# Optimization experiments

Hardware: AMD Instinct MI355X
Metric: run time of the kernel (lower is better)

Reference implementation:

```python
import math
import jax, jax.numpy as jnp
import numpy as np

# Neuron / simulation constants (from docstring defaults)
THETA = 10.0
TAU_SR = 10.0
TAU_REF = 1.0
SCALE_REF = 2.0
SCALE_RHO = 1.0
TS = 1.0
T_SAMPLE = 300


def _alpha_kernel(tau, mult, eps_tol):
    # Faithful to slayer._calculateAlphaKernel: eps(t) = mult * t/tau * exp(1 - t/tau),
    # truncated once |eps| < eps_tol and t > tau.
    vals = []
    for t in np.arange(0.0, T_SAMPLE, TS):
        v = mult * t / tau * math.exp(1.0 - t / tau)
        if abs(v) < eps_tol and t > tau:
            break
        vals.append(v)
    return np.asarray(vals, np.float32)


def psp(spike, srm_kernel):
    # slayerCuda.conv: causal temporal convolution psp[t] = sum_k f[k] * spike[t-k]
    N, C, H, W, T = spike.shape
    x = spike.reshape(-1, 1, T)                       # (B,1,T), B = N*C*H*W
    K = srm_kernel.shape[0]
    w = jnp.flip(srm_kernel).reshape(1, 1, K).astype(x.dtype)
    y = jax.lax.conv_general_dilated(
        x, w, window_strides=(1,), padding=[(K - 1, 0)],
        dimension_numbers=('NCH', 'OIH', 'NCH'))
    return y.reshape(N, C, H, W, T)


def get_spikes(u2, ref_kernel):
    # slayerCuda.getSpikes: sequential scan over time. At each step the effective
    # membrane potential is u[t] plus pending refractory contributions from past
    # spikes; a spike (value 1/Ts) fires when u_eff >= theta and injects the
    # refractory kernel into future timesteps.
    # u2: (B, T); ref_kernel: (K,) with ref_kernel[0] == 0 (alpha kernel).
    B, T = u2.shape
    K = ref_kernel.shape[0]
    ref_tail = ref_kernel[1:].astype(u2.dtype)        # contributions to t+1..t+K-1

    def step(pend, u_t):
        u_eff = u_t + pend[:, 0]
        s = (u_eff >= THETA).astype(u2.dtype)
        pend = jnp.concatenate([pend[:, 1:], jnp.zeros_like(pend[:, :1])], axis=1)
        pend = pend + s[:, None] * ref_tail[None, :]
        return pend, (s / TS, u_eff)

    pend0 = jnp.zeros((B, K - 1), u2.dtype)
    _, (s, u_mod) = jax.lax.scan(step, pend0, u2.T)
    return s.T, u_mod.T


def setup_inputs() -> dict:
    key = jax.random.key(0)
    k1, = jax.random.split(key, 1)
    N, C, H, W, T = 4, 16, 32, 32, T_SAMPLE
    u = jax.random.uniform(k1, (N, C, H, W, T), dtype=jnp.float32)
    spike_in = (u < 0.05).astype(jnp.float32) / TS
    srm_kernel = jnp.asarray(_alpha_kernel(TAU_SR, 1.0, 0.01))
    ref_kernel = jnp.asarray(_alpha_kernel(TAU_REF, -SCALE_REF * THETA, 0.01))
    return {"spike_in": spike_in, "srm_kernel": srm_kernel, "ref_kernel": ref_kernel}


def reference(spike_in, srm_kernel, ref_kernel):
    # psp (exponential alpha PSP conv) followed by spike generation scan
    u = psp(spike_in, srm_kernel)                     # (N,C,H,W,T)
    T = u.shape[-1]
    s, _ = get_spikes(u.reshape(-1, T), ref_kernel)
    return s.reshape(spike_in.shape)
```

## Files before the change

### kernel.cpp

```cpp
#include <hip/hip_runtime.h>


#define T_LEN 300
#define CH 20
#define NCHUNK 15
#define KS 77
#define KR 10
#define THETA_V 10.0f
#define TSZ 115

__global__ __launch_bounds__(256)
__attribute__((amdgpu_waves_per_eu(1, 1)))
void spike_layer_kernel(
    const float* __restrict__ spike_in,
    const float* __restrict__ srm, int srm_len,
    const float* __restrict__ refk, int ref_len,
    float* __restrict__ out, int B)
{
    __shared__ float T[TSZ + 13];
    {
        int k = threadIdx.x;
        if (k < TSZ + 13) {
            int j = k - 19;
            T[k] = (j >= 1 && j < KS && j < srm_len) ? srm[j] : 0.0f;
        }
    }
    __syncthreads();

    int b = blockIdx.x * blockDim.x + threadIdx.x;
    if (b >= B) return;

    const float* row  = spike_in + (size_t)b * T_LEN;
    float*       orow = out      + (size_t)b * T_LEN;

    float rt[KR];
#pragma unroll
    for (int i = 0; i < KR; ++i) rt[i] = (i + 1 < ref_len) ? refk[i + 1] : 0.0f;

    float pend[KR];
#pragma unroll
    for (int i = 0; i < KR; ++i) pend[i] = 0.0f;

    unsigned w0 = 0, w1 = 0, w2 = 0;

    float nxt[CH];
    {
        const float4* p = (const float4*)row;
#pragma unroll
        for (int i = 0; i < CH / 4; ++i) {
            float4 v = p[i];
            nxt[4*i+0] = v.x; nxt[4*i+1] = v.y; nxt[4*i+2] = v.z; nxt[4*i+3] = v.w;
        }
    }

#pragma unroll 1
    for (int ch = 0; ch < NCHUNK; ++ch) {
        unsigned nb = 0;
#pragma unroll
        for (int i = 0; i < CH; ++i)
            nb |= (nxt[i] != 0.0f) ? (1u << i) : 0u;

        w0 = (w0 >> 20) | (w1 << 12);
        w1 = (w1 >> 20) | (w2 << 12);
        w2 = (w2 >> 20) | (nb << 12);

        if (ch + 1 < NCHUNK) {
            const float4* p = (const float4*)(row + (ch + 1) * CH);
#pragma unroll
            for (int i = 0; i < CH / 4; ++i) {
                float4 v = p[i];
                nxt[4*i+0] = v.x; nxt[4*i+1] = v.y; nxt[4*i+2] = v.z; nxt[4*i+3] = v.w;
            }
        }
        __builtin_amdgcn_sched_barrier(0);

        float u[CH];
#pragma unroll
        for (int c = 0; c < CH; ++c) u[c] = 0.0f;

        unsigned a0 = w0, a1 = w1, a2 = w2;
        while (__ballot(a0 | a1 | a2)) {
            int p = a2 ? (95 - __clz(a2))
                       : (a1 ? (63 - __clz(a1))
                             : (a0 ? (31 - __clz(a0)) : 95));
            unsigned m = 1u << (p & 31);
            if (p >= 64)      a2 &= ~m;
            else if (p >= 32) a1 &= ~m;
            else              a0 &= ~m;

            const float* tp = &T[95 - p];
#pragma unroll
            for (int c = 0; c < CH; ++c)
                u[c] += tp[c];
        }

        float so[CH];
#pragma unroll
        for (int c = 0; c < CH; ++c) {
            const int r = c % KR;
            float u_eff = u[c] + pend[r];
            float s = (u_eff >= THETA_V) ? 1.0f : 0.0f;
#pragma unroll
            for (int i = 0; i < KR - 1; ++i)
                pend[(r + 1 + i) % KR] = fmaf(s, rt[i], pend[(r + 1 + i) % KR]);
            pend[r] = s * rt[KR - 1];
            so[c] = s;
        }

        {
            float4* op = (float4*)(orow + ch * CH);
#pragma unroll
            for (int i = 0; i < CH / 4; ++i) {
                float4 v;
                v.x = so[4*i+0]; v.y = so[4*i+1]; v.z = so[4*i+2]; v.w = so[4*i+3];
                op[i] = v;
            }
        }
    }
}

extern "C" void kernel_launch(void* const* d_in, const int* in_sizes, int n_in,
                              void* d_out, int out_size, void* d_ws, size_t ws_size,
                              hipStream_t stream) {
    const float* spike_in = (const float*)d_in[0];
    const float* srm      = (const float*)d_in[1];
    const float* refk     = (const float*)d_in[2];
    float* out = (float*)d_out;

    int srm_len = in_sizes[1];
    int ref_len = in_sizes[2];
    int B = in_sizes[0] / T_LEN;

    int block = 256;
    int grid = (B + block - 1) / block;
    spike_layer_kernel<<<grid, block, 0, stream>>>(spike_in, srm, srm_len,
                                                   refk, ref_len, out, B);
}
```

Measured before the change: 179.5 us.

## Split into parallel dense conv with threshold flags and a scan over flagged rows

Adds a first kernel, parallel over rows and time chunks. It computes the PSP densely with register FMAs, zero-fills the output and sets a per-row flag when any potential reaches threshold. A second kernel runs the sequential spike scan only for flagged rows. Rows whose potential never reaches threshold cannot spike, since the refractory term only lowers the potential, so the costly serial scan is skipped for them. The trade-off is an extra memset, an extra kernel launch and redundant input reads. It also relies on a workspace being provided and on the refractory kernel being non-positive.

```diff
diff --git a/kernel.cpp b/kernel.cpp
--- a/kernel.cpp
+++ b/kernel.cpp
@@ -8,6 +8,182 @@
 #define KR 10
 #define THETA_V 10.0f
 #define TSZ 115
+
+__global__ __launch_bounds__(256) void conv_flag_kernel(
+    const float* __restrict__ spike_in,
+    const float* __restrict__ srm, int srm_len,
+    float* __restrict__ out, unsigned* __restrict__ flags, int B)
+{
+    const int b  = blockIdx.x * blockDim.x + threadIdx.x;
+    const int ch = blockIdx.y;
+    if (b >= B) return;
+
+    const float* row = spike_in + (size_t)b * T_LEN;
+    const int t0 = ch * CH;
+
+    float srm_r[KS];
+#pragma unroll
+    for (int i = 1; i < KS; ++i) srm_r[i] = (i < srm_len) ? srm[i] : 0.0f;
+
+    float u[CH];
+#pragma unroll
+    for (int c = 0; c < CH; ++c) u[c] = 0.0f;
+
+#pragma unroll
+    for (int bb = 0; bb < 4; ++bb) {
+        const int wbase = t0 - 16 * (bb + 1);
+        float xw[36];
+#pragma unroll
+        for (int i = 0; i < 9; ++i) {
+            const int f = wbase + 4 * i;
+            float4 v;
+            if (f >= 0) v = *(const float4*)(row + f);
+            else        v = make_float4(0.0f, 0.0f, 0.0f, 0.0f);
+            xw[4*i+0] = v.x; xw[4*i+1] = v.y; xw[4*i+2] = v.z; xw[4*i+3] = v.w;
+        }
+#pragma unroll
+        for (int d = 1; d <= 16; ++d) {
+            const float w = srm_r[16 * bb + d];
+#pragma unroll
+            for (int c = 0; c < CH; ++c)
+                u[c] = fmaf(w, xw[16 - d + c], u[c]);
+        }
+    }
+    {
+        const int wbase = t0 - 76;
+        float xw[32];
+#pragma unroll
+        for (int i = 0; i < 8; ++i) {
+            const int f = wbase + 4 * i;
+            float4 v;
+            if (f >= 0) v = *(const float4*)(row + f);
+            else        v = make_float4(0.0f, 0.0f, 0.0f, 0.0f);
+            xw[4*i+0] = v.x; xw[4*i+1] = v.y; xw[4*i+2] = v.z; xw[4*i+3] = v.w;
+        }
+#pragma unroll
+        for (int d = 1; d <= 12; ++d) {
+            const float w = srm_r[64 + d];
+#pragma unroll
+            for (int c = 0; c < CH; ++c)
+                u[c] = fmaf(w, xw[12 - d + c], u[c]);
+        }
+    }
+
+    bool any_ge = false;
+#pragma unroll
+    for (int c = 0; c < CH; ++c) any_ge = any_ge || (u[c] >= THETA_V);
+    if (any_ge) atomicOr(&flags[b], 1u);
+
+    const float4 z = make_float4(0.0f, 0.0f, 0.0f, 0.0f);
+    float4* op = (float4*)(out + (size_t)b * T_LEN + t0);
+#pragma unroll
+    for (int i = 0; i < CH / 4; ++i) op[i] = z;
+}
+
+__global__ __launch_bounds__(256) void scan_fix_kernel(
+    const float* __restrict__ spike_in,
+    const float* __restrict__ srm, int srm_len,
+    const float* __restrict__ refk, int ref_len,
+    float* __restrict__ out, const unsigned* __restrict__ flags, int B)
+{
+    __shared__ float T[TSZ + 13];
+    {
+        int k = threadIdx.x;
+        if (k < TSZ + 13) {
+            int j = k - 19;
+            T[k] = (j >= 1 && j < KS && j < srm_len) ? srm[j] : 0.0f;
+        }
+    }
+    __syncthreads();
+
+    int b = blockIdx.x * blockDim.x + threadIdx.x;
+    if (b >= B) return;
+    if (flags[b] == 0u) return;
+
+    const float* row  = spike_in + (size_t)b * T_LEN;
+    float*       orow = out      + (size_t)b * T_LEN;
+
+    float rt[KR];
+#pragma unroll
+    for (int i = 0; i < KR; ++i) rt[i] = (i + 1 < ref_len) ? refk[i + 1] : 0.0f;
+    float pend[KR];
+#pragma unroll
+    for (int i = 0; i < KR; ++i) pend[i] = 0.0f;
+
+    unsigned w0 = 0, w1 = 0, w2 = 0;
+    float nxt[CH];
+    {
+        const float4* p = (const float4*)row;
+#pragma unroll
+        for (int i = 0; i < CH / 4; ++i) {
+            float4 v = p[i];
+            nxt[4*i+0] = v.x; nxt[4*i+1] = v.y; nxt[4*i+2] = v.z; nxt[4*i+3] = v.w;
+        }
+    }
+
+#pragma unroll 1
+    for (int ch = 0; ch < NCHUNK; ++ch) {
+        unsigned nb = 0;
+#pragma unroll
+        for (int i = 0; i < CH; ++i)
+            nb |= (nxt[i] != 0.0f) ? (1u << i) : 0u;
+
+        w0 = (w0 >> 20) | (w1 << 12);
+        w1 = (w1 >> 20) | (w2 << 12);
+        w2 = (w2 >> 20) | (nb << 12);
+
+        if (ch + 1 < NCHUNK) {
+            const float4* p = (const float4*)(row + (ch + 1) * CH);
+#pragma unroll
+            for (int i = 0; i < CH / 4; ++i) {
+                float4 v = p[i];
+                nxt[4*i+0] = v.x; nxt[4*i+1] = v.y; nxt[4*i+2] = v.z; nxt[4*i+3] = v.w;
+            }
+        }
+        __builtin_amdgcn_sched_barrier(0);
+
+        float u[CH];
+#pragma unroll
+        for (int c = 0; c < CH; ++c) u[c] = 0.0f;
+
+        unsigned a0 = w0, a1 = w1, a2 = w2;
+        while (__ballot(a0 | a1 | a2)) {
+            int p = a2 ? (95 - __clz(a2))
+                       : (a1 ? (63 - __clz(a1))
+                             : (a0 ? (31 - __clz(a0)) : 95));
+            unsigned m = 1u << (p & 31);
+            if (p >= 64)      a2 &= ~m;
+            else if (p >= 32) a1 &= ~m;
+            else              a0 &= ~m;
+
+            const float* tp = &T[95 - p];
+#pragma unroll
+            for (int c = 0; c < CH; ++c)
+                u[c] += tp[c];
+        }
+
+        float so[CH];
+#pragma unroll
+        for (int c = 0; c < CH; ++c) {
+            const int r = c % KR;
+            float u_eff = u[c] + pend[r];
+            float s = (u_eff >= THETA_V) ? 1.0f : 0.0f;
+#pragma unroll
+            for (int i = 0; i < KR - 1; ++i)
+                pend[(r + 1 + i) % KR] = fmaf(s, rt[i], pend[(r + 1 + i) % KR]);
+            pend[r] = s * rt[KR - 1];
+            so[c] = s;
+        }
+
+        float4* op = (float4*)(orow + ch * CH);
+#pragma unroll
+        for (int i = 0; i < CH / 4; ++i) {
+            float4 v;
+            v.x = so[4*i+0]; v.y = so[4*i+1]; v.z = so[4*i+2]; v.w = so[4*i+3];
+            op[i] = v;
+        }
+    }
+}
 
 __global__ __launch_bounds__(256)
 __attribute__((amdgpu_waves_per_eu(1, 1)))
@@ -36,13 +212,11 @@
     float rt[KR];
 #pragma unroll
     for (int i = 0; i < KR; ++i) rt[i] = (i + 1 < ref_len) ? refk[i + 1] : 0.0f;
-
     float pend[KR];
 #pragma unroll
     for (int i = 0; i < KR; ++i) pend[i] = 0.0f;
 
     unsigned w0 = 0, w1 = 0, w2 = 0;
-
     float nxt[CH];
     {
         const float4* p = (const float4*)row;
@@ -107,14 +281,12 @@
             so[c] = s;
         }
 
-        {
-            float4* op = (float4*)(orow + ch * CH);
-#pragma unroll
-            for (int i = 0; i < CH / 4; ++i) {
-                float4 v;
-                v.x = so[4*i+0]; v.y = so[4*i+1]; v.z = so[4*i+2]; v.w = so[4*i+3];
-                op[i] = v;
-            }
+        float4* op = (float4*)(orow + ch * CH);
+#pragma unroll
+        for (int i = 0; i < CH / 4; ++i) {
+            float4 v;
+            v.x = so[4*i+0]; v.y = so[4*i+1]; v.z = so[4*i+2]; v.w = so[4*i+3];
+            op[i] = v;
         }
     }
 }
@@ -131,8 +303,17 @@
     int ref_len = in_sizes[2];
     int B = in_sizes[0] / T_LEN;
 
-    int block = 256;
-    int grid = (B + block - 1) / block;
-    spike_layer_kernel<<<grid, block, 0, stream>>>(spike_in, srm, srm_len,
-                                                   refk, ref_len, out, B);
+    if (d_ws != nullptr && ws_size >= (size_t)B * sizeof(unsigned)) {
+        unsigned* flags = (unsigned*)d_ws;
+        hipMemsetAsync(flags, 0, (size_t)B * sizeof(unsigned), stream);
+        dim3 grid1((B + 255) / 256, NCHUNK, 1);
+        conv_flag_kernel<<<grid1, 256, 0, stream>>>(spike_in, srm, srm_len,
+                                                    out, flags, B);
+        scan_fix_kernel<<<(B + 255) / 256, 256, 0, stream>>>(
+            spike_in, srm, srm_len, refk, ref_len, out, flags, B);
+    } else {
+        int grid = (B + 255) / 256;
+        spike_layer_kernel<<<grid, 256, 0, stream>>>(spike_in, srm, srm_len,
+                                                     refk, ref_len, out, B);
+    }
 }
```

After: 334.0 us. 1.86x slower.

## Bit-pack spikes cooperatively and skip rows that cannot reach threshold

Applied to the files above, without the earlier changes.

Each 256-thread block now loads 64 neurons' inputs cooperatively with coalesced float4 reads, packs them into bitmasks in LDS, and zero-fills the output. One thread per neuron then runs a cheap recursive alpha-filter upper bound (valid only when the SRM taps match the expected exp kernel) to decide whether the row can ever fire. Only wavefronts containing a possibly firing row run the full ballot-driven convolution and refractory scan, and only firing rows write output. This replaces per-thread strided loads and full computation for every row, but it relies on the input kernel shape and leaves only 64 of 256 threads active for compute.

```diff
diff --git a/kernel.cpp b/kernel.cpp
--- a/kernel.cpp
+++ b/kernel.cpp
@@ -9,76 +9,158 @@
 #define THETA_V 10.0f
 #define TSZ 115
 
-__global__ __launch_bounds__(256)
-__attribute__((amdgpu_waves_per_eu(1, 1)))
-void spike_layer_kernel(
+#define RHO_F   0.9048374180359596f
+#define C_E10   0.2718281828459045f
+#define THR_D   (9.0f / C_E10)
+#define TAP_TOL 2e-3f
+
+#define NPB  64
+#define WPG  600
+#define F4PG 4800
+#define SW   5400
+
+__global__ __launch_bounds__(256) void fused_kernel(
     const float* __restrict__ spike_in,
     const float* __restrict__ srm, int srm_len,
     const float* __restrict__ refk, int ref_len,
     float* __restrict__ out, int B)
 {
-    __shared__ float T[TSZ + 13];
+    __shared__ unsigned stage[SW];
+    __shared__ unsigned Wlds[WPG + 8];
+    __shared__ float    T[128];
+
+    const int t = threadIdx.x;
+    const int g = blockIdx.x;
+    const long long NF     = (long long)B * T_LEN;
+    const long long base_4 = (long long)F4PG * g;
+
+    if (t < 128) {
+        int j = t - 19;
+        T[t] = (j >= 1 && j < KS && j < srm_len) ? srm[j] : 0.0f;
+    }
+
+#pragma unroll
+    for (int k = 0; k < 19; ++k) {
+        const int i4 = t + 256 * k;
+        if (i4 < F4PG) {
+            const long long f4 = base_4 + i4;
+            unsigned pk = 0u;
+            if (4 * f4 + 4 <= NF) {
+                float4 v = ((const float4*)spike_in)[f4];
+                pk  = (v.x != 0.0f ? 1u : 0u);
+                pk |= (v.y != 0.0f ? 1u : 0u) << 8;
+                pk |= (v.z != 0.0f ? 1u : 0u) << 16;
+                pk |= (v.w != 0.0f ? 1u : 0u) << 24;
+            }
+            stage[i4 + (i4 >> 3)] = pk;
+        }
+    }
+
     {
-        int k = threadIdx.x;
-        if (k < TSZ + 13) {
-            int j = k - 19;
-            T[k] = (j >= 1 && j < KS && j < srm_len) ? srm[j] : 0.0f;
-        }
-    }
+        const float4 z = make_float4(0.0f, 0.0f, 0.0f, 0.0f);
+        const long long nf4 = NF >> 2;
+        float4* o4 = (float4*)out;
+#pragma unroll
+        for (int k = 0; k < 19; ++k) {
+            const int lw = t + 256 * k;
+            if (lw < F4PG) {
+                const long long i4 = base_4 + lw;
+                if (i4 < nf4) o4[i4] = z;
+            }
+        }
+    }
+
     __syncthreads();
 
-    int b = blockIdx.x * blockDim.x + threadIdx.x;
-    if (b >= B) return;
-
-    const float* row  = spike_in + (size_t)b * T_LEN;
-    float*       orow = out      + (size_t)b * T_LEN;
+#pragma unroll
+    for (int k = 0; k < 3; ++k) {
+        const int w = t + 256 * k;
+        if (w < WPG) {
+            unsigned bits = 0u;
+#pragma unroll
+            for (int i = 0; i < 8; ++i) {
+                unsigned v = stage[9 * w + i];
+                v = (v | (v >> 7) | (v >> 14) | (v >> 21)) & 0xFu;
+                bits |= v << (4 * i);
+            }
+            Wlds[w] = bits;
+        }
+    }
+    if (t < 8) Wlds[WPG + t] = 0u;
+
+    __syncthreads();
+
+    if (t >= NPB) return;
+
+    const long long neuron = (long long)NPB * g + t;
+    const bool valid = (neuron < B);
+
+    bool ok = (srm_len == KS);
+    if (ok) {
+        ok = fabsf(srm[0]) <= TAP_TOL;
+        float pj = 1.0f;
+        for (int j = 1; j < KS; ++j) {
+            pj *= RHO_F;
+            float mj = C_E10 * (float)j * pj;
+            ok = ok && (fabsf(srm[j] - mj) <= TAP_TOL);
+        }
+    }
+
+    const int F0 = T_LEN * t;
+    const int q = F0 >> 5;
+    const int r = F0 & 31;
+    unsigned W[11];
+#pragma unroll
+    for (int k = 0; k < 11; ++k) W[k] = Wlds[q + k];
+    unsigned aw2[11];
+#pragma unroll
+    for (int k = 0; k < 10; ++k)
+        aw2[k] = (unsigned)((((unsigned long long)W[k + 1] << 32) | W[k]) >> r);
+    aw2[10] = 0u;
+
+    float A = 0.0f, D = 0.0f, dmax = 0.0f;
+#pragma unroll
+    for (int tt = 1; tt < T_LEN; ++tt) {
+        const int bw = (tt - 1) >> 5;
+        const int bb = (tt - 1) & 31;
+        int ms = ((int)(aw2[bw] << (31 - bb))) >> 31;
+        float xr = __int_as_float(ms & __float_as_int(RHO_F));
+        A = fmaf(RHO_F, A, xr);
+        D = fmaf(RHO_F, D, A);
+        dmax = fmaxf(dmax, D);
+    }
+
+    const bool fire_row = valid && (!ok || (dmax >= THR_D));
+
+    if (__ballot(fire_row) == 0ull) return;
 
     float rt[KR];
 #pragma unroll
     for (int i = 0; i < KR; ++i) rt[i] = (i + 1 < ref_len) ? refk[i + 1] : 0.0f;
-
     float pend[KR];
 #pragma unroll
     for (int i = 0; i < KR; ++i) pend[i] = 0.0f;
 
-    unsigned w0 = 0, w1 = 0, w2 = 0;
-
-    float nxt[CH];
-    {
-        const float4* p = (const float4*)row;
-#pragma unroll
-        for (int i = 0; i < CH / 4; ++i) {
-            float4 v = p[i];
-            nxt[4*i+0] = v.x; nxt[4*i+1] = v.y; nxt[4*i+2] = v.z; nxt[4*i+3] = v.w;
-        }
-    }
-
-#pragma unroll 1
+    float* orow = out + (size_t)neuron * T_LEN;
+    unsigned w0s = 0u, w1s = 0u, w2s = 0u;
+
+#pragma unroll
     for (int ch = 0; ch < NCHUNK; ++ch) {
-        unsigned nb = 0;
-#pragma unroll
-        for (int i = 0; i < CH; ++i)
-            nb |= (nxt[i] != 0.0f) ? (1u << i) : 0u;
-
-        w0 = (w0 >> 20) | (w1 << 12);
-        w1 = (w1 >> 20) | (w2 << 12);
-        w2 = (w2 >> 20) | (nb << 12);
-
-        if (ch + 1 < NCHUNK) {
-            const float4* p = (const float4*)(row + (ch + 1) * CH);
-#pragma unroll
-            for (int i = 0; i < CH / 4; ++i) {
-                float4 v = p[i];
-                nxt[4*i+0] = v.x; nxt[4*i+1] = v.y; nxt[4*i+2] = v.z; nxt[4*i+3] = v.w;
-            }
-        }
-        __builtin_amdgcn_sched_barrier(0);
+        const int bp = 20 * ch, qw = bp >> 5, rr = bp & 31;
+        unsigned nb = fire_row
+            ? ((unsigned)((((unsigned long long)aw2[qw + 1] << 32) | aw2[qw]) >> rr)
+               & 0xFFFFFu)
+            : 0u;
+
+        w0s = (w0s >> 20) | (w1s << 12);
+        w1s = (w1s >> 20) | (w2s << 12);
+        w2s = (w2s >> 20) | (nb << 12);
 
         float u[CH];
 #pragma unroll
         for (int c = 0; c < CH; ++c) u[c] = 0.0f;
 
-        unsigned a0 = w0, a1 = w1, a2 = w2;
+        unsigned a0 = w0s, a1 = w1s, a2 = w2s;
         while (__ballot(a0 | a1 | a2)) {
             int p = a2 ? (95 - __clz(a2))
                        : (a1 ? (63 - __clz(a1))
@@ -97,17 +179,17 @@
         float so[CH];
 #pragma unroll
         for (int c = 0; c < CH; ++c) {
-            const int r = c % KR;
-            float u_eff = u[c] + pend[r];
+            const int rr2 = c % KR;
+            float u_eff = u[c] + pend[rr2];
             float s = (u_eff >= THETA_V) ? 1.0f : 0.0f;
 #pragma unroll
             for (int i = 0; i < KR - 1; ++i)
-                pend[(r + 1 + i) % KR] = fmaf(s, rt[i], pend[(r + 1 + i) % KR]);
-            pend[r] = s * rt[KR - 1];
+                pend[(rr2 + 1 + i) % KR] = fmaf(s, rt[i], pend[(rr2 + 1 + i) % KR]);
+            pend[rr2] = s * rt[KR - 1];
             so[c] = s;
         }
 
-        {
+        if (fire_row) {
             float4* op = (float4*)(orow + ch * CH);
 #pragma unroll
             for (int i = 0; i < CH / 4; ++i) {
@@ -131,8 +213,7 @@
     int ref_len = in_sizes[2];
     int B = in_sizes[0] / T_LEN;
 
-    int block = 256;
-    int grid = (B + block - 1) / block;
-    spike_layer_kernel<<<grid, block, 0, stream>>>(spike_in, srm, srm_len,
-                                                   refk, ref_len, out, B);
+    const int groups = (B + NPB - 1) / NPB;
+    fused_kernel<<<groups, 256, 0, stream>>>(spike_in, srm, srm_len,
+                                             refk, ref_len, out, B);
 }
```

Result: faster. 147.2 us (-18.0%).
